# Optimization experiments

Measured on AMD Instinct MI355X. Metric: run time of the kernel, lower is better.

Reference implementation:

```python
import jax, jax.numpy as jnp
import numpy as np
import math

B, T, D, La, Lr = 8, 128, 512, 2, 2
H = La + Lr
DK = D // H  # 128
DFF = 4 * D


def _gelu(x):
    # BERT tanh-approx GELU, matching the torch module exactly
    return 0.5 * x * (1.0 + jnp.tanh(math.sqrt(2.0 / math.pi) * (x + 0.044715 * x ** 3)))


def _ln(x, g, b, eps=1e-5):
    mu = jnp.mean(x, axis=-1, keepdims=True)
    var = jnp.mean((x - mu) ** 2, axis=-1, keepdims=True)
    return (x - mu) * jax.lax.rsqrt(var + eps) * g + b


def setup_inputs() -> dict:
    key = jax.random.key(0)
    ks = jax.random.split(key, 16)
    n = lambda k, s, sc=1.0: jax.random.normal(k, s, dtype=jnp.float32) * sc
    return {
        'x': n(ks[0], (B, T, D)),
        'mask': jnp.ones((B, 1, T, T), dtype=jnp.int32),
        'abs_kernel': n(ks[1], (La, B, T, D)),
        'rel_kernel': n(ks[2], (Lr, B, T, T, D)),
        'Wc': n(ks[3], (3, D, D), 0.02), 'bc': jnp.zeros((3, D), jnp.float32),
        'Wpq': n(ks[4], (La, D, DK), 0.02), 'bpq': jnp.zeros((La, DK), jnp.float32),
        'Wpk': n(ks[5], (La, D, DK), 0.02), 'bpk': jnp.zeros((La, DK), jnp.float32),
        'Wrk': n(ks[6], (Lr, D, DK), 0.02), 'brk': jnp.zeros((Lr, DK), jnp.float32),
        'rel_bias': n(ks[7], (Lr, DK), 0.02),
        'Wo': n(ks[8], (D, D), 0.02), 'bo': jnp.zeros((D,), jnp.float32),
        'W1': n(ks[9], (D, DFF), 0.02), 'b1': jnp.zeros((DFF,), jnp.float32),
        'W2': n(ks[10], (DFF, D), 0.02), 'b2': jnp.zeros((D,), jnp.float32),
        'ln1_g': jnp.ones((D,), jnp.float32), 'ln1_b': jnp.zeros((D,), jnp.float32),
        'ln2_g': jnp.ones((D,), jnp.float32), 'ln2_b': jnp.zeros((D,), jnp.float32),
    }


def _attention(h, mask, abs_kernel, rel_kernel, Wc, bc, Wpq, bpq, Wpk, bpk,
               Wrk, brk, rel_bias, Wo, bo):
    b, t = h.shape[0], h.shape[1]
    # content projections: [3,B,T,D] -> [3,B,H,T,DK]
    qkv = jnp.einsum('btd,cde->cbte', h, Wc) + bc[:, None, None, :]
    qkv = qkv.reshape(3, b, t, H, DK).transpose(0, 1, 3, 2, 4)
    q, k, v = qkv[0], qkv[1], qkv[2]
    # absolute-position heads
    Pq = jnp.einsum('abtd,ade->bate', abs_kernel, Wpq) + bpq[None, :, None, :]
    Pk = jnp.einsum('abtd,ade->bate', abs_kernel, Wpk) + bpk[None, :, None, :]
    abs_scores = jnp.einsum('blid,bljd->blij', q[:, :La] + Pq, k[:, :La] + Pk)
    # relative-position heads (R: [B,Lr,T,T,DK])
    R = jnp.einsum('abijd,ade->baije', rel_kernel, Wrk) + brk[None, :, None, None, :]
    Xq = q[:, La:]
    rel_scores = jnp.einsum('blid,bljd->blij', Xq, k[:, La:])
    rel_scores = rel_scores + jnp.einsum('blid,blijd->blij', Xq + rel_bias[None, :, None, :], R)
    scores = jnp.concatenate([abs_scores, rel_scores], axis=1) * (DK ** -0.5)
    scores = jnp.where(mask == 0, jnp.float32(-1e9), scores)
    p_attn = jax.nn.softmax(scores, axis=-1)
    out = jnp.einsum('bhij,bhjd->bhid', p_attn, v)
    out = out.transpose(0, 2, 1, 3).reshape(b, t, H * DK)
    return out @ Wo + bo


def reference(x, mask, abs_kernel, rel_kernel, Wc, bc, Wpq, bpq, Wpk, bpk,
              Wrk, brk, rel_bias, Wo, bo, W1, b1, W2, b2,
              ln1_g, ln1_b, ln2_g, ln2_b):
    # pre-LN sublayer 1: attention
    h = _ln(x, ln1_g, ln1_b)
    x = x + _attention(h, mask, abs_kernel, rel_kernel, Wc, bc, Wpq, bpq,
                       Wpk, bpk, Wrk, brk, rel_bias, Wo, bo)
    # pre-LN sublayer 2: FFN with tanh-GELU
    h2 = _ln(x, ln2_g, ln2_b)
    x = x + (_gelu(h2 @ W1 + b1) @ W2 + b2)
    return x
```

## Files before the change

### kernel.cpp

```cpp
#include <hip/hip_runtime.h>
#include <math.h>

typedef __attribute__((ext_vector_type(8))) short short8v;
typedef __attribute__((ext_vector_type(4))) float f32x4;

static __device__ __forceinline__ ushort f2bf(float x) {
  unsigned u = __builtin_bit_cast(unsigned, x);
  unsigned r = (u + 0x7fffu + ((u >> 16) & 1u)) >> 16;
  return (ushort)r;
}

__device__ __forceinline__ float gelu_f(float v) {
  float t = tanhf(0.7978845608028654f * (v + 0.044715f * v * v * v));
  return 0.5f * v * (1.0f + t);
}

__device__ __forceinline__ void transpose_tile(char* shm,
    const float* __restrict__ src, ushort* __restrict__ dst,
    int R, int C, int lb)
{
  ushort (*tile)[65] = (ushort(*)[65])shm;
  int t = threadIdx.x;
  int tpr = C >> 6;
  int tyy = lb / tpr, txx = lb - tyy * tpr;
  int r0 = tyy << 6, c0 = txx << 6;
  int lr = t >> 4, lc4 = (t & 15) << 2;
  #pragma unroll
  for (int i = 0; i < 4; ++i) {
    int row = i*16 + lr;
    float4 vv = *(const float4*)(src + (size_t)(r0+row)*C + c0 + lc4);
    tile[row][lc4+0] = f2bf(vv.x);
    tile[row][lc4+1] = f2bf(vv.y);
    tile[row][lc4+2] = f2bf(vv.z);
    tile[row][lc4+3] = f2bf(vv.w);
  }
  __syncthreads();
  #pragma unroll
  for (int i = 0; i < 4; ++i) {
    int n = i*16 + lr;
    ushort4 o;
    o.x = tile[lc4+0][n];
    o.y = tile[lc4+1][n];
    o.z = tile[lc4+2][n];
    o.w = tile[lc4+3][n];
    *(ushort4*)(dst + (size_t)(c0+n)*R + r0 + lc4) = o;
  }
}

struct CvtTasks {
  const float* src[16];
  void* dst[16];
  int rows[16], cols[16], mode[16], aux[16], end[16];
};

__global__ __launch_bounds__(256) void cvt_kernel(CvtTasks T,
    const float* __restrict__ lnx, const float* __restrict__ lng,
    const float* __restrict__ lnb, ushort* __restrict__ lnout)
{
  __shared__ __align__(16) char shm[8448];
  int b = blockIdx.x, t = threadIdx.x;
  int ti = 0;
  while (b >= T.end[ti]) ++ti;
  int lb = b - (ti ? T.end[ti-1] : 0);
  const float* src = T.src[ti];
  int mode = T.mode[ti];
  if (mode == 0) {
    transpose_tile(shm, src, (ushort*)T.dst[ti], T.rows[ti], T.cols[ti], lb);
  } else if (mode == 1) {
    int idx = lb*2048 + t*8;
    float4 v0 = *(const float4*)(src + idx);
    float4 v1 = *(const float4*)(src + idx + 4);
    union { ushort u[8]; uint4 q; } pk;
    pk.u[0]=f2bf(v0.x); pk.u[1]=f2bf(v0.y); pk.u[2]=f2bf(v0.z); pk.u[3]=f2bf(v0.w);
    pk.u[4]=f2bf(v1.x); pk.u[5]=f2bf(v1.y); pk.u[6]=f2bf(v1.z); pk.u[7]=f2bf(v1.w);
    *(uint4*)((ushort*)T.dst[ti] + idx) = pk.q;
  } else if (mode == 2) {
    if (t < T.cols[ti]) {
      float* d = (float*)T.dst[ti];
      for (int r = 0; r < T.rows[ti]; ++r)
        d[(size_t)(2*r + T.aux[ti]) * T.cols[ti] + t] = src[(size_t)r * T.cols[ti] + t];
    }
  } else {
    int row = lb*4 + (t >> 6);
    int lane = t & 63;
    const float* xr = lnx + (size_t)row*512 + lane*8;
    float4 a = *(const float4*)xr;
    float4 c = *(const float4*)(xr + 4);
    float s  = a.x + a.y + a.z + a.w + c.x + c.y + c.z + c.w;
    float ss = a.x*a.x + a.y*a.y + a.z*a.z + a.w*a.w
             + c.x*c.x + c.y*c.y + c.z*c.z + c.w*c.w;
    #pragma unroll
    for (int off = 32; off > 0; off >>= 1) {
      s  += __shfl_xor(s, off);
      ss += __shfl_xor(ss, off);
    }
    float mu  = s * (1.0f/512.0f);
    float var = ss * (1.0f/512.0f) - mu*mu;
    float rstd = rsqrtf(var + 1e-5f);
    float4 g0 = *(const float4*)(lng + lane*8), g1 = *(const float4*)(lng + lane*8 + 4);
    float4 b0 = *(const float4*)(lnb + lane*8), b1 = *(const float4*)(lnb + lane*8 + 4);
    union { ushort u[8]; uint4 v; } pk;
    pk.u[0] = f2bf((a.x-mu)*rstd*g0.x + b0.x);
    pk.u[1] = f2bf((a.y-mu)*rstd*g0.y + b0.y);
    pk.u[2] = f2bf((a.z-mu)*rstd*g0.z + b0.z);
    pk.u[3] = f2bf((a.w-mu)*rstd*g0.w + b0.w);
    pk.u[4] = f2bf((c.x-mu)*rstd*g1.x + b1.x);
    pk.u[5] = f2bf((c.y-mu)*rstd*g1.y + b1.y);
    pk.u[6] = f2bf((c.z-mu)*rstd*g1.z + b1.z);
    pk.u[7] = f2bf((c.w-mu)*rstd*g1.w + b1.w);
    *(uint4*)(lnout + (size_t)row*512 + lane*8) = pk.v;
  }
}

template<bool OUT_BF16, bool GELU_>
__device__ __forceinline__ void gemm64_body(char* smem,
    const ushort* __restrict__ A, int lda,
    const ushort* __restrict__ Bt, int ldb,
    const float* __restrict__ bias,
    void* __restrict__ Cout, int ldc,
    int ksteps, int bm, int bn)
{
  int tid = threadIdx.x;
  int lane = tid & 63, wid = tid >> 6;
  int wr = wid >> 1, wc = wid & 1;
  int l15 = lane & 15, kg = lane >> 4;
  f32x4 acc[2][2] = {};
  const ushort* Ab = A + (size_t)bm * lda;
  const ushort* Bb = Bt + (size_t)bn * ldb;
  int r0 = tid >> 3;
  int c16 = tid & 7;
  int wb0 = r0*128 + ((c16*16) ^ ((r0 & 7) << 4));
  int wb1 = (r0+32)*128 + ((c16*16) ^ ((r0 & 7) << 4));
  uint4 ra0 = *(const uint4*)(Ab + (size_t)r0*lda + c16*8);
  uint4 ra1 = *(const uint4*)(Ab + (size_t)(r0+32)*lda + c16*8);
  uint4 rb0 = *(const uint4*)(Bb + (size_t)r0*ldb + c16*8);
  uint4 rb1 = *(const uint4*)(Bb + (size_t)(r0+32)*ldb + c16*8);
  *(uint4*)(smem + wb0) = ra0;  *(uint4*)(smem + wb1) = ra1;
  *(uint4*)(smem + 8192 + wb0) = rb0;  *(uint4*)(smem + 8192 + wb1) = rb1;
  __syncthreads();
  for (int ks = 0; ks < ksteps; ++ks) {
    char* buf = smem + (ks & 1)*16384;
    char* nxt = smem + ((ks + 1) & 1)*16384;
    bool more = (ks + 1 < ksteps);
    if (more) {
      int k0 = (ks + 1) * 64;
      ra0 = *(const uint4*)(Ab + (size_t)r0*lda + k0 + c16*8);
      ra1 = *(const uint4*)(Ab + (size_t)(r0+32)*lda + k0 + c16*8);
      rb0 = *(const uint4*)(Bb + (size_t)r0*ldb + k0 + c16*8);
      rb1 = *(const uint4*)(Bb + (size_t)(r0+32)*ldb + k0 + c16*8);
    }
    char* asB = buf;
    char* bsB = buf + 8192;
    #pragma unroll
    for (int half = 0; half < 2; ++half) {
      int cb = half*64 + kg*16;
      short8v av[2], bv[2];
      #pragma unroll
      for (int m = 0; m < 2; ++m) {
        int r = wr*32 + m*16 + l15;
        av[m] = *(const short8v*)(asB + r*128 + (cb ^ ((r & 7) << 4)));
      }
      #pragma unroll
      for (int n = 0; n < 2; ++n) {
        int r = wc*32 + n*16 + l15;
        bv[n] = *(const short8v*)(bsB + r*128 + (cb ^ ((r & 7) << 4)));
      }
      #pragma unroll
      for (int m = 0; m < 2; ++m)
        #pragma unroll
        for (int n = 0; n < 2; ++n)
          acc[m][n] = __builtin_amdgcn_mfma_f32_16x16x32_bf16(av[m], bv[n], acc[m][n], 0, 0, 0);
    }
    if (more) {
      *(uint4*)(nxt + wb0) = ra0;  *(uint4*)(nxt + wb1) = ra1;
      *(uint4*)(nxt + 8192 + wb0) = rb0;  *(uint4*)(nxt + 8192 + wb1) = rb1;
    }
    __syncthreads();
  }
  int orow0 = bm + wr*32 + kg*4;
  int ocol0 = bn + wc*32 + l15;
  #pragma unroll
  for (int m = 0; m < 2; ++m) {
    #pragma unroll
    for (int r = 0; r < 4; ++r) {
      int row = orow0 + m*16 + r;
      #pragma unroll
      for (int n = 0; n < 2; ++n) {
        int col = ocol0 + n*16;
        float val = acc[m][n][r];
        if (bias) val += bias[col];
        if (GELU_) val = gelu_f(val);
        if (OUT_BF16) ((ushort*)Cout)[(size_t)row*ldc + col] = f2bf(val);
        else          ((float*)Cout)[(size_t)row*ldc + col]  = val;
      }
    }
  }
}

template<bool OUT_BF16, bool GELU_>
__global__ __launch_bounds__(256) void g64(
    const ushort* __restrict__ A, int lda, long Abatch,
    const ushort* __restrict__ Bt, int ldb, long Bbatch,
    const float* __restrict__ bias, int biasStride,
    void* __restrict__ C, int ldc, long Cbatch,
    int ksteps)
{
  __shared__ __align__(16) char smem[32768];
  int z = blockIdx.z;
  const float* bz = bias ? bias + (size_t)z * biasStride : nullptr;
  void* Cz = OUT_BF16 ? (void*)((ushort*)C + (size_t)z*Cbatch)
                      : (void*)((float*)C + (size_t)z*Cbatch);
  gemm64_body<OUT_BF16, GELU_>(smem, A + (size_t)z*Abatch, lda,
      Bt + (size_t)z*Bbatch, ldb, bz, Cz, ldc, ksteps,
      blockIdx.y*64, blockIdx.x*64);
}

__global__ __launch_bounds__(256) void qkvp_gemm(
    const ushort* __restrict__ h, const ushort* __restrict__ WcT,
    const float* __restrict__ bc, float* __restrict__ qkv,
    const ushort* __restrict__ absb, const ushort* __restrict__ Wp,
    const float* __restrict__ bqk, float* __restrict__ Pqk)
{
  __shared__ __align__(16) char smem[32768];
  int z = blockIdx.z;
  const ushort *A, *Bt;
  const float* bias;
  float* C;
  int ldc;
  if (z < 3) {
    A = h; Bt = WcT + (size_t)z*262144; bias = bc + z*512;
    C = qkv + (size_t)z*524288; ldc = 512;
  } else {
    if (blockIdx.x >= 2) return;
    int t = z - 3;
    A = absb + (size_t)(t >> 1)*524288;
    Bt = Wp + (size_t)t*65536;
    bias = bqk + t*128;
    C = Pqk + (size_t)t*131072; ldc = 128;
  }
  gemm64_body<false,false>(smem, A, 512, Bt, 512, bias, C, ldc, 8,
      blockIdx.y*64, blockIdx.x*64);
}

__global__ __launch_bounds__(256) void fused_pre(
    const float* __restrict__ q, const float* __restrict__ k,
    float* __restrict__ Pqk, const float* __restrict__ rel_bias,
    const float* __restrict__ brk, const ushort* __restrict__ Wrkb,
    float* __restrict__ u, float* __restrict__ cvec)
{
  int blk = blockIdx.x;
  int tid = threadIdx.x;
  if (blk < 256) {
    int l = blk >> 7;
    int rem = blk & 127;
    int bm = (rem >> 3) * 64;
    int bn = (rem & 7) * 64;
    __shared__ __align__(16) char smem[16384];
    char* asB = smem;
    char* bsB = smem + 8192;
    int lane = tid & 63, wid = tid >> 6;
    int wr = wid >> 1, wc = wid & 1;
    int l15 = lane & 15, kg = lane >> 4;
    f32x4 acc[2][2] = {};
    const ushort* Bb = Wrkb + (size_t)l*65536 + (size_t)bn*128;
    int r0 = tid >> 3, c16 = tid & 7;
    int wb0 = r0*128 + ((c16*16) ^ ((r0 & 7) << 4));
    int wb1 = (r0+32)*128 + ((c16*16) ^ ((r0 & 7) << 4));
    const float* rbp = rel_bias + l*128;
    #pragma unroll
    for (int ks = 0; ks < 2; ++ks) {
      int k0 = ks * 64;
      int e0 = k0 + c16*8;
      uint4 ra[2], rb[2];
      #pragma unroll
      for (int i = 0; i < 2; ++i) {
        int m = bm + r0 + i*32;
        const float* qp = q + (size_t)m*512 + (2+l)*128 + e0;
        float4 qa = *(const float4*)qp;
        float4 qb = *(const float4*)(qp + 4);
        float4 rr0 = *(const float4*)(rbp + e0);
        float4 rr1 = *(const float4*)(rbp + e0 + 4);
        union { ushort s[8]; uint4 v; } pk;
        pk.s[0]=f2bf(qa.x+rr0.x); pk.s[1]=f2bf(qa.y+rr0.y);
        pk.s[2]=f2bf(qa.z+rr0.z); pk.s[3]=f2bf(qa.w+rr0.w);
        pk.s[4]=f2bf(qb.x+rr1.x); pk.s[5]=f2bf(qb.y+rr1.y);
        pk.s[6]=f2bf(qb.z+rr1.z); pk.s[7]=f2bf(qb.w+rr1.w);
        ra[i] = pk.v;
        rb[i] = *(const uint4*)(Bb + (size_t)(r0 + i*32)*128 + k0 + c16*8);
      }
      __syncthreads();
      *(uint4*)(asB + wb0) = ra[0];  *(uint4*)(asB + wb1) = ra[1];
      *(uint4*)(bsB + wb0) = rb[0];  *(uint4*)(bsB + wb1) = rb[1];
      __syncthreads();
      #pragma unroll
      for (int half = 0; half < 2; ++half) {
        int cb = half*64 + kg*16;
        short8v av[2], bv[2];
        #pragma unroll
        for (int m = 0; m < 2; ++m) {
          int r = wr*32 + m*16 + l15;
          av[m] = *(const short8v*)(asB + r*128 + (cb ^ ((r & 7) << 4)));
        }
        #pragma unroll
        for (int n = 0; n < 2; ++n) {
          int r = wc*32 + n*16 + l15;
          bv[n] = *(const short8v*)(bsB + r*128 + (cb ^ ((r & 7) << 4)));
        }
        #pragma unroll
        for (int m = 0; m < 2; ++m)
          #pragma unroll
          for (int n = 0; n < 2; ++n)
            acc[m][n] = __builtin_amdgcn_mfma_f32_16x16x32_bf16(av[m], bv[n], acc[m][n], 0, 0, 0);
      }
    }
    float* Cz = u + (size_t)l*524288;
    int orow0 = bm + wr*32 + kg*4;
    int ocol0 = bn + wc*32 + l15;
    #pragma unroll
    for (int m = 0; m < 2; ++m)
      #pragma unroll
      for (int r = 0; r < 4; ++r) {
        int row = orow0 + m*16 + r;
        #pragma unroll
        for (int n = 0; n < 2; ++n)
          Cz[(size_t)row*512 + ocol0 + n*16] = acc[m][n][r];
      }
  } else if (blk < 1280) {
    int idx = (blk - 256)*256 + tid;
    int dk = idx & 127;
    int rest = idx >> 7;
    int m = rest & 1023;
    int a = rest >> 10;
    Pqk[idx + a*131072]     += q[(size_t)m*512 + a*128 + dk];
    Pqk[idx + (a+1)*131072] += k[(size_t)m*512 + a*128 + dk];
  } else {
    int row = (blk - 1280)*2 + (tid >> 7);
    int l = row >> 10, m = row & 1023;
    int t = tid & 127, hf = tid >> 7;
    float val = q[(size_t)m*512 + (2+l)*128 + t] + rel_bias[l*128 + t];
    float p = brk[l*128 + t] * val;
    #pragma unroll
    for (int off = 32; off > 0; off >>= 1) p += __shfl_xor(p, off);
    __shared__ float red[2][2];
    if ((tid & 63) == 0) red[hf][(tid >> 6) & 1] = p;
    __syncthreads();
    if (t == 0) cvec[row] = red[hf][0] + red[hf][1];
  }
}

__global__ __launch_bounds__(256) void attn_kernel(
    const float* __restrict__ rk, const float* __restrict__ u,
    const float* __restrict__ q, const float* __restrict__ k,
    const float* __restrict__ v, const float* __restrict__ cvec,
    const float* __restrict__ Pqk, const int* __restrict__ mask,
    ushort* __restrict__ attnob,
    const float* __restrict__ Wo, ushort* __restrict__ WoT,
    const float* __restrict__ W1, ushort* __restrict__ W1T,
    const float* __restrict__ W2, ushort* __restrict__ W2T)
{
  __shared__ __align__(16) char shm[8448];
  int blk = blockIdx.x;
  int tid = threadIdx.x;
  if (blk < 2048) {
    struct RelShm { float qs[128], sc[128], ps[128], red[64], pvs[2][128], stat[2]; };
    RelShm* S = (RelShm*)shm;
    int i = blk & 127, b = (blk >> 7) & 7, l = blk >> 10, h = 2 + l;
    int m_i = b*128 + i;
    int wave = tid >> 6, lane = tid & 63;
    const float* ur = u + ((size_t)l*1024 + m_i)*512 + lane*8;
    float4 uu0 = *(const float4*)ur;
    float4 uu1 = *(const float4*)(ur + 4);
    if (tid < 128) S->qs[tid] = q[(size_t)m_i*512 + h*128 + tid];
    __syncthreads();
    float xq0 = S->qs[lane*2], xq1 = S->qs[lane*2+1];
    const float* base = rk + (size_t)blk*65536 + lane*8;
    const float* kb = k + (size_t)(b*128)*512 + h*128 + lane*2;
    #pragma unroll 2
    for (int jj = 0; jj < 32; ++jj) {
      int j = wave*32 + jj;
      const float* r = base + (size_t)j*512;
      float4 r0 = *(const float4*)r;
      float4 r1 = *(const float4*)(r + 4);
      float2 kk = *(const float2*)(kb + (size_t)j*512);
      float s = r0.x*uu0.x + r0.y*uu0.y + r0.z*uu0.z + r0.w*uu0.w
              + r1.x*uu1.x + r1.y*uu1.y + r1.z*uu1.z + r1.w*uu1.w
              + kk.x*xq0 + kk.y*xq1;
      #pragma unroll
      for (int off = 32; off > 0; off >>= 1) s += __shfl_xor(s, off);
      if (lane == 0) S->sc[j] = s;
    }
    __syncthreads();
    if (tid < 128) {
      float sv = (S->sc[tid] + cvec[l*1024 + m_i]) * 0.088388347648318447f;
      if (mask[((size_t)(b*128) + i)*128 + tid] == 0) sv = -1e9f;
      S->sc[tid] = sv;
    }
    __syncthreads();
    if (tid < 64) S->red[tid] = fmaxf(S->sc[tid], S->sc[tid+64]);
    __syncthreads();
    if (tid < 64) {
      float m = S->red[tid];
      #pragma unroll
      for (int off = 32; off > 0; off >>= 1) m = fmaxf(m, __shfl_xor(m, off));
      if (tid == 0) S->stat[0] = m;
    }
    __syncthreads();
    if (tid < 128) S->ps[tid] = __expf(S->sc[tid] - S->stat[0]);
    __syncthreads();
    if (tid < 64) S->red[tid] = S->ps[tid] + S->ps[tid+64];
    __syncthreads();
    if (tid < 64) {
      float s = S->red[tid];
      #pragma unroll
      for (int off = 32; off > 0; off >>= 1) s += __shfl_xor(s, off);
      if (tid == 0) S->stat[1] = 1.0f / s;
    }
    __syncthreads();
    int hf = tid >> 7, dk = tid & 127;
    const float* vp = v + (size_t)(b*128 + hf*64)*512 + h*128 + dk;
    float o = 0.0f;
    #pragma unroll 4
    for (int jj = 0; jj < 64; ++jj) o += S->ps[hf*64 + jj] * vp[(size_t)jj*512];
    S->pvs[hf][dk] = o;
    __syncthreads();
    if (tid < 128)
      attnob[(size_t)m_i*512 + h*128 + tid] = f2bf((S->pvs[0][tid] + S->pvs[1][tid]) * S->stat[1]);
  } else if (blk < 3072) {
    struct AbsShm { float qsh[2][128], psh[2][128], redm[2][2], reds[2][2]; };
    AbsShm* S = (AbsShm*)shm;
    int ab = blk - 2048;
    int hf = tid >> 7, t = tid & 127;
    int i  = (ab & 63)*2 + hf;
    int bh = ab >> 6;
    int h  = bh & 1, b = bh >> 1;
    int m_i = b*128 + i;
    S->qsh[hf][t] = Pqk[(size_t)(2*h)*131072 + (size_t)m_i*128 + t];
    __syncthreads();
    int m_j = b*128 + t;
    const float* krow = Pqk + (size_t)(2*h+1)*131072 + (size_t)m_j*128;
    float dot = 0.0f;
    #pragma unroll
    for (int d = 0; d < 128; d += 4) {
      float4 kv = *(const float4*)(krow + d);
      dot += kv.x*S->qsh[hf][d] + kv.y*S->qsh[hf][d+1] + kv.z*S->qsh[hf][d+2] + kv.w*S->qsh[hf][d+3];
    }
    float s = dot * 0.088388347648318447f;
    if (mask[((size_t)(b*128) + i)*128 + t] == 0) s = -1e9f;
    float mx = s;
    #pragma unroll
    for (int off = 32; off > 0; off >>= 1) mx = fmaxf(mx, __shfl_xor(mx, off));
    int w2 = (tid >> 6) & 1;
    if ((tid & 63) == 0) S->redm[hf][w2] = mx;
    __syncthreads();
    mx = fmaxf(S->redm[hf][0], S->redm[hf][1]);
    float e = __expf(s - mx);
    S->psh[hf][t] = e;
    float sum = e;
    #pragma unroll
    for (int off = 32; off > 0; off >>= 1) sum += __shfl_xor(sum, off);
    if ((tid & 63) == 0) S->reds[hf][w2] = sum;
    __syncthreads();
    float inv = 1.0f / (S->reds[hf][0] + S->reds[hf][1]);
    const float* vp = v + (size_t)b*65536 + h*128 + t;
    float o = 0.0f;
    #pragma unroll 4
    for (int jj = 0; jj < 128; ++jj) o += S->psh[hf][jj] * vp[(size_t)jj*512];
    attnob[(size_t)m_i*512 + h*128 + t] = f2bf(o * inv);
  } else {
    int t2 = blk - 3072;
    if (t2 < 64)       transpose_tile(shm, Wo, WoT, 512, 512, t2);
    else if (t2 < 320) transpose_tile(shm, W1, W1T, 512, 2048, t2 - 64);
    else               transpose_tile(shm, W2, W2T, 2048, 512, t2 - 320);
  }
}

__global__ __launch_bounds__(256) void reduce_ln_kernel(
    const float* __restrict__ wpart, const float* __restrict__ bo,
    const float* __restrict__ x, const float* __restrict__ g,
    const float* __restrict__ bb, float* __restrict__ x1,
    ushort* __restrict__ h2)
{
  int gid = blockIdx.x*256 + threadIdx.x;
  int row = gid >> 6, lane = threadIdx.x & 63;
  size_t off = (size_t)row*512 + lane*8;
  float4 a = *(const float4*)(x + off);
  float4 c = *(const float4*)(x + off + 4);
  #pragma unroll
  for (int sk = 0; sk < 4; ++sk) {
    float4 p0 = *(const float4*)(wpart + (size_t)sk*524288 + off);
    float4 p1 = *(const float4*)(wpart + (size_t)sk*524288 + off + 4);
    a.x += p0.x; a.y += p0.y; a.z += p0.z; a.w += p0.w;
    c.x += p1.x; c.y += p1.y; c.z += p1.z; c.w += p1.w;
  }
  float4 bo0 = *(const float4*)(bo + lane*8);
  float4 bo1 = *(const float4*)(bo + lane*8 + 4);
  a.x += bo0.x; a.y += bo0.y; a.z += bo0.z; a.w += bo0.w;
  c.x += bo1.x; c.y += bo1.y; c.z += bo1.z; c.w += bo1.w;
  *(float4*)(x1 + off) = a;
  *(float4*)(x1 + off + 4) = c;
  float s  = a.x + a.y + a.z + a.w + c.x + c.y + c.z + c.w;
  float ss = a.x*a.x + a.y*a.y + a.z*a.z + a.w*a.w
           + c.x*c.x + c.y*c.y + c.z*c.z + c.w*c.w;
  #pragma unroll
  for (int off2 = 32; off2 > 0; off2 >>= 1) {
    s  += __shfl_xor(s, off2);
    ss += __shfl_xor(ss, off2);
  }
  float mu  = s * (1.0f/512.0f);
  float var = ss * (1.0f/512.0f) - mu*mu;
  float rstd = rsqrtf(var + 1e-5f);
  float4 g0 = *(const float4*)(g + lane*8), g1 = *(const float4*)(g + lane*8 + 4);
  float4 b0 = *(const float4*)(bb + lane*8), b1 = *(const float4*)(bb + lane*8 + 4);
  union { ushort u[8]; uint4 v; } pk;
  pk.u[0] = f2bf((a.x-mu)*rstd*g0.x + b0.x);
  pk.u[1] = f2bf((a.y-mu)*rstd*g0.y + b0.y);
  pk.u[2] = f2bf((a.z-mu)*rstd*g0.z + b0.z);
  pk.u[3] = f2bf((a.w-mu)*rstd*g0.w + b0.w);
  pk.u[4] = f2bf((c.x-mu)*rstd*g1.x + b1.x);
  pk.u[5] = f2bf((c.y-mu)*rstd*g1.y + b1.y);
  pk.u[6] = f2bf((c.z-mu)*rstd*g1.z + b1.z);
  pk.u[7] = f2bf((c.w-mu)*rstd*g1.w + b1.w);
  *(uint4*)(h2 + off) = pk.v;
}

__global__ __launch_bounds__(256) void reduce_out_kernel(
    const float* __restrict__ fpart, const float* __restrict__ b2,
    const float* __restrict__ x1, float* __restrict__ out)
{
  int idx = blockIdx.x*256 + threadIdx.x;
  size_t o4 = (size_t)idx*4;
  float4 s = *(const float4*)(x1 + o4);
  #pragma unroll
  for (int sk = 0; sk < 4; ++sk) {
    float4 p = *(const float4*)(fpart + (size_t)sk*524288 + o4);
    s.x += p.x; s.y += p.y; s.z += p.z; s.w += p.w;
  }
  float4 bv = *(const float4*)(b2 + ((idx & 127)*4));
  s.x += bv.x; s.y += bv.y; s.z += bv.z; s.w += bv.w;
  *(float4*)(out + o4) = s;
}

extern "C" void kernel_launch(void* const* d_in, const int* in_sizes, int n_in,
                              void* d_out, int out_size, void* d_ws, size_t ws_size,
                              hipStream_t stream)
{
  const float* x         = (const float*)d_in[0];
  const int*   mask      = (const int*)  d_in[1];
  const float* abs_kernel= (const float*)d_in[2];
  const float* rel_kernel= (const float*)d_in[3];
  const float* Wc        = (const float*)d_in[4];
  const float* bc        = (const float*)d_in[5];
  const float* Wpq       = (const float*)d_in[6];
  const float* bpq       = (const float*)d_in[7];
  const float* Wpk       = (const float*)d_in[8];
  const float* bpk       = (const float*)d_in[9];
  const float* Wrk       = (const float*)d_in[10];
  const float* brk       = (const float*)d_in[11];
  const float* rel_bias  = (const float*)d_in[12];
  const float* Wo        = (const float*)d_in[13];
  const float* bo        = (const float*)d_in[14];
  const float* W1        = (const float*)d_in[15];
  const float* b1        = (const float*)d_in[16];
  const float* W2        = (const float*)d_in[17];
  const float* b2        = (const float*)d_in[18];
  const float* ln1g      = (const float*)d_in[19];
  const float* ln1b      = (const float*)d_in[20];
  const float* ln2g      = (const float*)d_in[21];
  const float* ln2b      = (const float*)d_in[22];

  float* ws = (float*)d_ws;
  float* q      = ws;
  float* kbuf   = ws + 524288;
  float* v      = ws + 1048576;
  float* Pqk    = ws + 1572864;
  float* u      = ws + 2097152;
  float* x1     = ws + 3145728;
  float* cvec   = ws + 3670016;
  float* bqk    = ws + 3672064;
  float* wpart  = ws + 3672576;
  float* fpart  = wpart;
  ushort* bf    = (ushort*)(ws + 5769728);
  ushort* h     = bf;
  ushort* h2    = bf + 524288;
  ushort* attnob= bf + 1048576;
  ushort* f1    = bf + 1572864;
  ushort* absb  = bf + 3670016;
  ushort* WcT   = bf + 4718592;
  ushort* Wp    = bf + 5505024;
  ushort* Wrkb  = bf + 5767168;
  ushort* WoT   = bf + 5898240;
  ushort* W1T   = bf + 6160384;
  ushort* W2T   = bf + 7208960;
  float* out    = (float*)d_out;

  CvtTasks T{};
  int nb = 0, ti = 0;
  auto addTr = [&](const float* s, ushort* d, int R, int C) {
    T.src[ti]=s; T.dst[ti]=d; T.rows[ti]=R; T.cols[ti]=C; T.mode[ti]=0; T.aux[ti]=0;
    nb += (R/64)*(C/64); T.end[ti]=nb; ++ti;
  };
  auto addCv = [&](const float* s, ushort* d, int n) {
    T.src[ti]=s; T.dst[ti]=d; T.rows[ti]=n; T.cols[ti]=0; T.mode[ti]=1; T.aux[ti]=0;
    nb += n/2048; T.end[ti]=nb; ++ti;
  };
  auto addBi = [&](const float* s, float* d, int aux) {
    T.src[ti]=s; T.dst[ti]=d; T.rows[ti]=2; T.cols[ti]=128; T.mode[ti]=2; T.aux[ti]=aux;
    nb += 1; T.end[ti]=nb; ++ti;
  };
  for (int c = 0; c < 3; ++c) addTr(Wc + (size_t)c*262144, WcT + (size_t)c*262144, 512, 512);
  for (int a = 0; a < 2; ++a) addTr(Wpq + (size_t)a*65536, Wp + (size_t)(2*a)*65536, 512, 128);
  for (int a = 0; a < 2; ++a) addTr(Wpk + (size_t)a*65536, Wp + (size_t)(2*a+1)*65536, 512, 128);
  addCv(abs_kernel, absb, 1048576);
  addCv(Wrk, Wrkb, 131072);
  addBi(bpq, bqk, 0);
  addBi(bpk, bqk, 1);
  T.src[ti]=x; T.dst[ti]=h; T.mode[ti]=3; nb += 256; T.end[ti]=nb; ++ti;

  cvt_kernel<<<nb, 256, 0, stream>>>(T, x, ln1g, ln1b, h);

  qkvp_gemm<<<dim3(8,16,7), 256, 0, stream>>>(h, WcT, bc, q, absb, Wp, bqk, Pqk);

  fused_pre<<<2304, 256, 0, stream>>>(q, kbuf, Pqk, rel_bias, brk, Wrkb, u, cvec);

  attn_kernel<<<3648, 256, 0, stream>>>(rel_kernel, u, q, kbuf, v, cvec, Pqk,
                                        mask, attnob, Wo, WoT, W1, W1T, W2, W2T);

  g64<false,false><<<dim3(8,16,4), 256, 0, stream>>>(
      attnob, 512, 128, WoT, 512, 128, nullptr, 0, wpart, 512, 524288, 2);

  reduce_ln_kernel<<<256, 256, 0, stream>>>(wpart, bo, x, ln2g, ln2b, x1, h2);

  g64<true,true><<<dim3(32,16,1), 256, 0, stream>>>(
      h2, 512, 0, W1T, 512, 0, b1, 0, f1, 2048, 0, 8);

  g64<false,false><<<dim3(8,16,4), 256, 0, stream>>>(
      f1, 2048, 512, W2T, 2048, 512, nullptr, 0, fpart, 512, 524288, 8);

  reduce_out_kernel<<<512, 256, 0, stream>>>(fpart, b2, x1, out);
}
```

Before: 197.7 us.

## Fuse LN1 normalize and fp32-to-bf16 conversions into GEMM A/B loads

The pre-pass kernel now computes only the per-row LayerNorm statistics instead of writing a normalized bf16 copy of x. The normalization and bf16 packing move into the QKV GEMM's A-tile loader through a templated load functor. abs_kernel and Wrk are likewise no longer pre-converted to bf16 and are converted on the fly inside qkvp_gemm and fused_pre. This removes intermediate bf16 buffers and their write/read traffic, at the cost of redundant conversion work and wider fp32 global loads in the GEMM inner loops, since each A tile is re-read by every column block.

```diff
diff --git a/kernel.cpp b/kernel.cpp
--- a/kernel.cpp
+++ b/kernel.cpp
@@ -54,8 +54,7 @@
 };
 
 __global__ __launch_bounds__(256) void cvt_kernel(CvtTasks T,
-    const float* __restrict__ lnx, const float* __restrict__ lng,
-    const float* __restrict__ lnb, ushort* __restrict__ lnout)
+    const float* __restrict__ lnx, float2* __restrict__ stats)
 {
   __shared__ __align__(16) char shm[8448];
   int b = blockIdx.x, t = threadIdx.x;
@@ -66,14 +65,6 @@
   int mode = T.mode[ti];
   if (mode == 0) {
     transpose_tile(shm, src, (ushort*)T.dst[ti], T.rows[ti], T.cols[ti], lb);
-  } else if (mode == 1) {
-    int idx = lb*2048 + t*8;
-    float4 v0 = *(const float4*)(src + idx);
-    float4 v1 = *(const float4*)(src + idx + 4);
-    union { ushort u[8]; uint4 q; } pk;
-    pk.u[0]=f2bf(v0.x); pk.u[1]=f2bf(v0.y); pk.u[2]=f2bf(v0.z); pk.u[3]=f2bf(v0.w);
-    pk.u[4]=f2bf(v1.x); pk.u[5]=f2bf(v1.y); pk.u[6]=f2bf(v1.z); pk.u[7]=f2bf(v1.w);
-    *(uint4*)((ushort*)T.dst[ti] + idx) = pk.q;
   } else if (mode == 2) {
     if (t < T.cols[ti]) {
       float* d = (float*)T.dst[ti];
@@ -96,25 +87,54 @@
     }
     float mu  = s * (1.0f/512.0f);
     float var = ss * (1.0f/512.0f) - mu*mu;
-    float rstd = rsqrtf(var + 1e-5f);
-    float4 g0 = *(const float4*)(lng + lane*8), g1 = *(const float4*)(lng + lane*8 + 4);
-    float4 b0 = *(const float4*)(lnb + lane*8), b1 = *(const float4*)(lnb + lane*8 + 4);
-    union { ushort u[8]; uint4 v; } pk;
-    pk.u[0] = f2bf((a.x-mu)*rstd*g0.x + b0.x);
-    pk.u[1] = f2bf((a.y-mu)*rstd*g0.y + b0.y);
-    pk.u[2] = f2bf((a.z-mu)*rstd*g0.z + b0.z);
-    pk.u[3] = f2bf((a.w-mu)*rstd*g0.w + b0.w);
-    pk.u[4] = f2bf((c.x-mu)*rstd*g1.x + b1.x);
-    pk.u[5] = f2bf((c.y-mu)*rstd*g1.y + b1.y);
-    pk.u[6] = f2bf((c.z-mu)*rstd*g1.z + b1.z);
-    pk.u[7] = f2bf((c.w-mu)*rstd*g1.w + b1.w);
-    *(uint4*)(lnout + (size_t)row*512 + lane*8) = pk.v;
-  }
-}
-
-template<bool OUT_BF16, bool GELU_>
-__device__ __forceinline__ void gemm64_body(char* smem,
-    const ushort* __restrict__ A, int lda,
+    if (lane == 0) stats[row] = make_float2(mu, rsqrtf(var + 1e-5f));
+  }
+}
+
+struct LoadBf16 {
+  const ushort* Ab; int lda;
+  __device__ __forceinline__ uint4 operator()(int r, int e) const {
+    return *(const uint4*)(Ab + (size_t)r*lda + e);
+  }
+};
+
+struct LoadLN {
+  const float* x0;
+  const float2* st0;
+  const float* g; const float* bb;
+  __device__ __forceinline__ uint4 operator()(int r, int e) const {
+    const float* xp = x0 + (size_t)r*512 + e;
+    float4 xa = *(const float4*)xp, xb = *(const float4*)(xp + 4);
+    float2 st = st0[r];
+    float4 ga = *(const float4*)(g + e),  gb = *(const float4*)(g + e + 4);
+    float4 ba = *(const float4*)(bb + e), bv = *(const float4*)(bb + e + 4);
+    union { ushort s[8]; uint4 v; } pk;
+    pk.s[0]=f2bf((xa.x-st.x)*st.y*ga.x+ba.x);
+    pk.s[1]=f2bf((xa.y-st.x)*st.y*ga.y+ba.y);
+    pk.s[2]=f2bf((xa.z-st.x)*st.y*ga.z+ba.z);
+    pk.s[3]=f2bf((xa.w-st.x)*st.y*ga.w+ba.w);
+    pk.s[4]=f2bf((xb.x-st.x)*st.y*gb.x+bv.x);
+    pk.s[5]=f2bf((xb.y-st.x)*st.y*gb.y+bv.y);
+    pk.s[6]=f2bf((xb.z-st.x)*st.y*gb.z+bv.z);
+    pk.s[7]=f2bf((xb.w-st.x)*st.y*gb.w+bv.w);
+    return pk.v;
+  }
+};
+
+struct LoadCvt {
+  const float* A; int lda;
+  __device__ __forceinline__ uint4 operator()(int r, int e) const {
+    const float* p = A + (size_t)r*lda + e;
+    float4 a = *(const float4*)p, b = *(const float4*)(p + 4);
+    union { ushort s[8]; uint4 v; } pk;
+    pk.s[0]=f2bf(a.x); pk.s[1]=f2bf(a.y); pk.s[2]=f2bf(a.z); pk.s[3]=f2bf(a.w);
+    pk.s[4]=f2bf(b.x); pk.s[5]=f2bf(b.y); pk.s[6]=f2bf(b.z); pk.s[7]=f2bf(b.w);
+    return pk.v;
+  }
+};
+
+template<bool OUT_BF16, bool GELU_, class LA>
+__device__ __forceinline__ void gemm64_dbuf(char* smem, const LA& loadA,
     const ushort* __restrict__ Bt, int ldb,
     const float* __restrict__ bias,
     void* __restrict__ Cout, int ldc,
@@ -125,14 +145,13 @@
   int wr = wid >> 1, wc = wid & 1;
   int l15 = lane & 15, kg = lane >> 4;
   f32x4 acc[2][2] = {};
-  const ushort* Ab = A + (size_t)bm * lda;
   const ushort* Bb = Bt + (size_t)bn * ldb;
   int r0 = tid >> 3;
   int c16 = tid & 7;
   int wb0 = r0*128 + ((c16*16) ^ ((r0 & 7) << 4));
   int wb1 = (r0+32)*128 + ((c16*16) ^ ((r0 & 7) << 4));
-  uint4 ra0 = *(const uint4*)(Ab + (size_t)r0*lda + c16*8);
-  uint4 ra1 = *(const uint4*)(Ab + (size_t)(r0+32)*lda + c16*8);
+  uint4 ra0 = loadA(r0, c16*8);
+  uint4 ra1 = loadA(r0+32, c16*8);
   uint4 rb0 = *(const uint4*)(Bb + (size_t)r0*ldb + c16*8);
   uint4 rb1 = *(const uint4*)(Bb + (size_t)(r0+32)*ldb + c16*8);
   *(uint4*)(smem + wb0) = ra0;  *(uint4*)(smem + wb1) = ra1;
@@ -144,8 +163,8 @@
     bool more = (ks + 1 < ksteps);
     if (more) {
       int k0 = (ks + 1) * 64;
-      ra0 = *(const uint4*)(Ab + (size_t)r0*lda + k0 + c16*8);
-      ra1 = *(const uint4*)(Ab + (size_t)(r0+32)*lda + k0 + c16*8);
+      ra0 = loadA(r0, k0 + c16*8);
+      ra1 = loadA(r0+32, k0 + c16*8);
       rb0 = *(const uint4*)(Bb + (size_t)r0*ldb + k0 + c16*8);
       rb1 = *(const uint4*)(Bb + (size_t)(r0+32)*ldb + k0 + c16*8);
     }
@@ -207,45 +226,43 @@
 {
   __shared__ __align__(16) char smem[32768];
   int z = blockIdx.z;
+  int bm = blockIdx.y*64, bn = blockIdx.x*64;
   const float* bz = bias ? bias + (size_t)z * biasStride : nullptr;
   void* Cz = OUT_BF16 ? (void*)((ushort*)C + (size_t)z*Cbatch)
                       : (void*)((float*)C + (size_t)z*Cbatch);
-  gemm64_body<OUT_BF16, GELU_>(smem, A + (size_t)z*Abatch, lda,
-      Bt + (size_t)z*Bbatch, ldb, bz, Cz, ldc, ksteps,
-      blockIdx.y*64, blockIdx.x*64);
+  LoadBf16 la{ A + (size_t)z*Abatch + (size_t)bm*lda, lda };
+  gemm64_dbuf<OUT_BF16, GELU_>(smem, la, Bt + (size_t)z*Bbatch, ldb, bz,
+      Cz, ldc, ksteps, bm, bn);
 }
 
 __global__ __launch_bounds__(256) void qkvp_gemm(
-    const ushort* __restrict__ h, const ushort* __restrict__ WcT,
-    const float* __restrict__ bc, float* __restrict__ qkv,
-    const ushort* __restrict__ absb, const ushort* __restrict__ Wp,
-    const float* __restrict__ bqk, float* __restrict__ Pqk)
+    const float* __restrict__ x, const float2* __restrict__ stats,
+    const float* __restrict__ ln1g, const float* __restrict__ ln1b,
+    const ushort* __restrict__ WcT, const float* __restrict__ bc,
+    float* __restrict__ qkv, const float* __restrict__ abs_kernel,
+    const ushort* __restrict__ Wp, const float* __restrict__ bqk,
+    float* __restrict__ Pqk)
 {
   __shared__ __align__(16) char smem[32768];
   int z = blockIdx.z;
-  const ushort *A, *Bt;
-  const float* bias;
-  float* C;
-  int ldc;
+  int bm = blockIdx.y*64, bn = blockIdx.x*64;
   if (z < 3) {
-    A = h; Bt = WcT + (size_t)z*262144; bias = bc + z*512;
-    C = qkv + (size_t)z*524288; ldc = 512;
+    LoadLN la{ x + (size_t)bm*512, stats + bm, ln1g, ln1b };
+    gemm64_dbuf<false,false>(smem, la, WcT + (size_t)z*262144, 512,
+        bc + z*512, qkv + (size_t)z*524288, 512, 8, bm, bn);
   } else {
     if (blockIdx.x >= 2) return;
     int t = z - 3;
-    A = absb + (size_t)(t >> 1)*524288;
-    Bt = Wp + (size_t)t*65536;
-    bias = bqk + t*128;
-    C = Pqk + (size_t)t*131072; ldc = 128;
-  }
-  gemm64_body<false,false>(smem, A, 512, Bt, 512, bias, C, ldc, 8,
-      blockIdx.y*64, blockIdx.x*64);
+    LoadCvt la{ abs_kernel + (size_t)(t >> 1)*524288 + (size_t)bm*512, 512 };
+    gemm64_dbuf<false,false>(smem, la, Wp + (size_t)t*65536, 512,
+        bqk + t*128, Pqk + (size_t)t*131072, 128, 8, bm, bn);
+  }
 }
 
 __global__ __launch_bounds__(256) void fused_pre(
     const float* __restrict__ q, const float* __restrict__ k,
     float* __restrict__ Pqk, const float* __restrict__ rel_bias,
-    const float* __restrict__ brk, const ushort* __restrict__ Wrkb,
+    const float* __restrict__ brk, const float* __restrict__ Wrk,
     float* __restrict__ u, float* __restrict__ cvec)
 {
   int blk = blockIdx.x;
@@ -262,7 +279,7 @@
     int wr = wid >> 1, wc = wid & 1;
     int l15 = lane & 15, kg = lane >> 4;
     f32x4 acc[2][2] = {};
-    const ushort* Bb = Wrkb + (size_t)l*65536 + (size_t)bn*128;
+    const float* Bb = Wrk + (size_t)l*65536 + (size_t)bn*128;
     int r0 = tid >> 3, c16 = tid & 7;
     int wb0 = r0*128 + ((c16*16) ^ ((r0 & 7) << 4));
     int wb1 = (r0+32)*128 + ((c16*16) ^ ((r0 & 7) << 4));
@@ -286,7 +303,15 @@
         pk.s[4]=f2bf(qb.x+rr1.x); pk.s[5]=f2bf(qb.y+rr1.y);
         pk.s[6]=f2bf(qb.z+rr1.z); pk.s[7]=f2bf(qb.w+rr1.w);
         ra[i] = pk.v;
-        rb[i] = *(const uint4*)(Bb + (size_t)(r0 + i*32)*128 + k0 + c16*8);
+        const float* bp = Bb + (size_t)(r0 + i*32)*128 + e0;
+        float4 b0 = *(const float4*)bp;
+        float4 b1 = *(const float4*)(bp + 4);
+        union { ushort s[8]; uint4 v; } pkb;
+        pkb.s[0]=f2bf(b0.x); pkb.s[1]=f2bf(b0.y);
+        pkb.s[2]=f2bf(b0.z); pkb.s[3]=f2bf(b0.w);
+        pkb.s[4]=f2bf(b1.x); pkb.s[5]=f2bf(b1.y);
+        pkb.s[6]=f2bf(b1.z); pkb.s[7]=f2bf(b1.w);
+        rb[i] = pkb.v;
       }
       __syncthreads();
       *(uint4*)(asB + wb0) = ra[0];  *(uint4*)(asB + wb1) = ra[1];
@@ -577,20 +602,18 @@
   float* x1     = ws + 3145728;
   float* cvec   = ws + 3670016;
   float* bqk    = ws + 3672064;
-  float* wpart  = ws + 3672576;
+  float2* stats = (float2*)(ws + 3672576);
+  float* wpart  = ws + 3674624;
   float* fpart  = wpart;
-  ushort* bf    = (ushort*)(ws + 5769728);
-  ushort* h     = bf;
-  ushort* h2    = bf + 524288;
-  ushort* attnob= bf + 1048576;
-  ushort* f1    = bf + 1572864;
-  ushort* absb  = bf + 3670016;
-  ushort* WcT   = bf + 4718592;
-  ushort* Wp    = bf + 5505024;
-  ushort* Wrkb  = bf + 5767168;
-  ushort* WoT   = bf + 5898240;
-  ushort* W1T   = bf + 6160384;
-  ushort* W2T   = bf + 7208960;
+  ushort* bf    = (ushort*)(ws + 5771776);
+  ushort* h2    = bf;
+  ushort* attnob= bf + 524288;
+  ushort* f1    = bf + 1048576;
+  ushort* WcT   = bf + 3145728;
+  ushort* Wp    = bf + 3932160;
+  ushort* WoT   = bf + 4194304;
+  ushort* W1T   = bf + 4456448;
+  ushort* W2T   = bf + 5505024;
   float* out    = (float*)d_out;
 
   CvtTasks T{};
@@ -598,10 +621,6 @@
   auto addTr = [&](const float* s, ushort* d, int R, int C) {
     T.src[ti]=s; T.dst[ti]=d; T.rows[ti]=R; T.cols[ti]=C; T.mode[ti]=0; T.aux[ti]=0;
     nb += (R/64)*(C/64); T.end[ti]=nb; ++ti;
-  };
-  auto addCv = [&](const float* s, ushort* d, int n) {
-    T.src[ti]=s; T.dst[ti]=d; T.rows[ti]=n; T.cols[ti]=0; T.mode[ti]=1; T.aux[ti]=0;
-    nb += n/2048; T.end[ti]=nb; ++ti;
   };
   auto addBi = [&](const float* s, float* d, int aux) {
     T.src[ti]=s; T.dst[ti]=d; T.rows[ti]=2; T.cols[ti]=128; T.mode[ti]=2; T.aux[ti]=aux;
@@ -610,17 +629,16 @@
   for (int c = 0; c < 3; ++c) addTr(Wc + (size_t)c*262144, WcT + (size_t)c*262144, 512, 512);
   for (int a = 0; a < 2; ++a) addTr(Wpq + (size_t)a*65536, Wp + (size_t)(2*a)*65536, 512, 128);
   for (int a = 0; a < 2; ++a) addTr(Wpk + (size_t)a*65536, Wp + (size_t)(2*a+1)*65536, 512, 128);
-  addCv(abs_kernel, absb, 1048576);
-  addCv(Wrk, Wrkb, 131072);
   addBi(bpq, bqk, 0);
   addBi(bpk, bqk, 1);
-  T.src[ti]=x; T.dst[ti]=h; T.mode[ti]=3; nb += 256; T.end[ti]=nb; ++ti;
-
-  cvt_kernel<<<nb, 256, 0, stream>>>(T, x, ln1g, ln1b, h);
-
-  qkvp_gemm<<<dim3(8,16,7), 256, 0, stream>>>(h, WcT, bc, q, absb, Wp, bqk, Pqk);
-
-  fused_pre<<<2304, 256, 0, stream>>>(q, kbuf, Pqk, rel_bias, brk, Wrkb, u, cvec);
+  T.src[ti]=x; T.dst[ti]=nullptr; T.mode[ti]=3; nb += 256; T.end[ti]=nb; ++ti;
+
+  cvt_kernel<<<nb, 256, 0, stream>>>(T, x, stats);
+
+  qkvp_gemm<<<dim3(8,16,7), 256, 0, stream>>>(x, stats, ln1g, ln1b, WcT, bc,
+                                              q, abs_kernel, Wp, bqk, Pqk);
+
+  fused_pre<<<2304, 256, 0, stream>>>(q, kbuf, Pqk, rel_bias, brk, Wrk, u, cvec);
 
   attn_kernel<<<3648, 256, 0, stream>>>(rel_kernel, u, q, kbuf, v, cvec, Pqk,
                                         mask, attnob, Wo, WoT, W1, W1T, W2, W2T);
```

After: 203.5 us. 1.03x slower.
